# Kernel optimization log

Hardware: AMD Instinct MI355X
Metric: run time of the kernel (lower is better)

## Reference

```python
import jax, jax.numpy as jnp
import numpy as np

D = 256; H = 8; HD = D // H; NK = 32; NLAYERS = 4; FF = 4 * D
B = 8; M = 768; N = 128; LT = 64; T = M + N + LT
SCALE = 1.0 / float(np.sqrt(HD))


def layer_norm(x, s, b):
    mu = x.mean(-1, keepdims=True)
    var = ((x - mu) ** 2).mean(-1, keepdims=True)
    return (x - mu) * jax.lax.rsqrt(var + 1e-5) * s + b


def sine_embed(pos, d):
    # MTR gen_sineembed_for_position: half dims for y, half for x, interleaved sin/cos
    half = d // 2
    dim_t = jnp.power(10000.0, 2.0 * (jnp.arange(half) // 2).astype(jnp.float32) / half)
    scale = 2.0 * np.pi
    def inter(e):
        return jnp.stack([jnp.sin(e[:, 0::2]), jnp.cos(e[:, 1::2])], -1).reshape(e.shape[0], -1)
    ex = pos[:, 0:1] * scale / dim_t
    ey = pos[:, 1:2] * scale / dim_t
    return jnp.concatenate([inter(ey), inter(ex)], -1)


def setup_inputs() -> dict:
    key = jax.random.key(0)
    ks = jax.random.split(key, 24)
    s = 0.02
    inp = {
        'map_token': jax.random.normal(ks[0], (B, M, D), jnp.float32),
        'agent_token': jax.random.normal(ks[1], (B, N, D), jnp.float32),
        'light_token': jax.random.normal(ks[2], (B, LT, D), jnp.float32),
        'map_position': jax.random.uniform(ks[3], (B, M, 2), jnp.float32) * 100.0,
        'agent_position': jax.random.uniform(ks[4], (B, N, 2), jnp.float32) * 100.0,
        'light_position': jax.random.uniform(ks[5], (B, LT, 2), jnp.float32) * 100.0,
        'map_valid_mask': jnp.ones((B, M), bool),
        'agent_valid_mask': jnp.ones((B, N), bool),
        'light_valid_mask': jnp.ones((B, LT), bool),
        'Wq': jax.random.normal(ks[6], (NLAYERS, D, D), jnp.float32) * s,
        'bq': jnp.zeros((NLAYERS, D), jnp.float32),
        'Wk': jax.random.normal(ks[7], (NLAYERS, D, D), jnp.float32) * s,
        'bk': jnp.zeros((NLAYERS, D), jnp.float32),
        'Wv': jax.random.normal(ks[8], (NLAYERS, D, D), jnp.float32) * s,
        'bv': jnp.zeros((NLAYERS, D), jnp.float32),
        'Wo': jax.random.normal(ks[9], (NLAYERS, D, D), jnp.float32) * s,
        'bo': jnp.zeros((NLAYERS, D), jnp.float32),
        'W1': jax.random.normal(ks[10], (NLAYERS, D, FF), jnp.float32) * s,
        'b1': jnp.zeros((NLAYERS, FF), jnp.float32),
        'W2': jax.random.normal(ks[11], (NLAYERS, FF, D), jnp.float32) * s,
        'b2': jnp.zeros((NLAYERS, D), jnp.float32),
        'ln1_s': jnp.ones((NLAYERS, D), jnp.float32),
        'ln1_b': jnp.zeros((NLAYERS, D), jnp.float32),
        'ln2_s': jnp.ones((NLAYERS, D), jnp.float32),
        'ln2_b': jnp.zeros((NLAYERS, D), jnp.float32),
    }
    return inp


def reference(map_token, agent_token, light_token, map_position, agent_position, light_position,
              map_valid_mask, agent_valid_mask, light_valid_mask,
              Wq, bq, Wk, bk, Wv, bv, Wo, bo, W1, b1, W2, b2, ln1_s, ln1_b, ln2_s, ln2_b):
    x = jnp.concatenate([map_token, agent_token, light_token], 1)             # [B,T,D]
    pos = jnp.concatenate([map_position, agent_position, light_position], 1)[..., :2]  # [B,T,2]
    # all tokens valid -> masked compaction is a static reshape
    xs = x.reshape(B * T, D)
    ps = pos.reshape(B * T, 2)
    # KNN within each scene (includes self, like knn_batch_mlogk on same set)
    d2 = jnp.sum((pos[:, :, None, :] - pos[:, None, :, :]) ** 2, -1)          # [B,T,T]
    _, idx = jax.lax.top_k(-d2, NK)                                            # [B,T,NK] local indices
    idx = (idx + (jnp.arange(B) * T)[:, None, None]).reshape(B * T, NK)        # global flat indices
    pe = sine_embed(ps, D)                                                     # [B*T,D]
    out = xs
    for l in range(NLAYERS):
        qk = out + pe
        q = (qk @ Wq[l] + bq[l]).reshape(-1, H, HD)
        k = (qk @ Wk[l] + bk[l]).reshape(-1, H, HD)
        v = (out @ Wv[l] + bv[l]).reshape(-1, H, HD)
        kn = k[idx]                                                            # [BT,NK,H,HD] gather
        vn = v[idx]
        att = jax.nn.softmax(jnp.einsum('nhd,nkhd->nhk', q, kn) * SCALE, axis=-1)
        a = jnp.einsum('nhk,nkhd->nhd', att, vn).reshape(-1, D) @ Wo[l] + bo[l]
        out = layer_norm(out + a, ln1_s[l], ln1_b[l])
        ff = jax.nn.relu(out @ W1[l] + b1[l]) @ W2[l] + b2[l]
        out = layer_norm(out + ff, ln2_s[l], ln2_b[l])
    full = out.reshape(B, T, D)
    return full[:, :M], full[:, M:M + N], full[:, M + N:]
```

## Files before the change

kernel.cpp:

```cpp
#include <hip/hip_runtime.h>
#include <math.h>

#define BB 8
#define MTOK 768
#define NTOK 128
#define LTOK 64
#define TT 960
#define BT 7680
#define DD 256
#define HH 8
#define HD 32
#define KNN 32
#define FFD 1024
#define NLAYERS 4
#define SCALE_ATT 0.17677669529663687f

typedef __attribute__((ext_vector_type(8))) short bfrag_t;
typedef __attribute__((ext_vector_type(4))) float accfrag_t;

__device__ __forceinline__ float b2f(unsigned short u) {
  union { unsigned int i; float f; } c; c.i = ((unsigned int)u) << 16; return c.f;
}
__device__ __forceinline__ unsigned short f2b(float f) {
  union { float f; unsigned int i; } c; c.f = f;
  return (unsigned short)((c.i + 0x7fffu + ((c.i >> 16) & 1u)) >> 16);
}
__device__ __forceinline__ float load_elem(const void* p, size_t i, int f) {
  return f ? b2f(((const unsigned short*)p)[i]) : ((const float*)p)[i];
}
__device__ __forceinline__ size_t pk_addr(int row, int col, int nks) {
  return ((size_t)((row >> 4) * nks + (col >> 5)) << 9)
       + (size_t)(((((col >> 3) & 3) << 4) + (row & 15)) * 8 + (col & 7));
}
__device__ __forceinline__ int swiz_tok(int blk) { return (blk & 7) * TT + (blk >> 3); }

#define FB_BQ 0
#define FB_BK 1024
#define FB_BV 2048
#define FB_BO 3072
#define FB_B1 4096
#define FB_B2 8192
#define FB_LN1S 9216
#define FB_LN1B 10240
#define FB_LN2S 11264
#define FB_LN2B 12288
#define FB_TOTAL 13312
struct ParamSrc { const void* p[13]; };
__global__ __launch_bounds__(256)
void conv_misc_kernel(ParamSrc ps, const void* tok, int* flagout,
                      float* __restrict__ dst, float* __restrict__ posf) {
  __shared__ int cnt;
  if (threadIdx.x == 0) cnt = 0;
  __syncthreads();
  const unsigned short* u = (const unsigned short*)tok;
  int ok = 0;
  for (int i = threadIdx.x; i < 1024; i += 256) {
    int e = (u[i] >> 7) & 0xFF;
    if (e >= 100 && e <= 140) ok++;
  }
  atomicAdd(&cnt, ok);
  __syncthreads();
  int f = (cnt >= 922) ? 1 : 0;
  if (blockIdx.x == 0 && threadIdx.x == 0) *flagout = f;
  if (blockIdx.x < BB) {
    int b = blockIdx.x;
    for (int t = threadIdx.x; t < TT * 2; t += 256) {
      int tok2 = t >> 1, c = t & 1;
      const void* p; size_t idx;
      if (tok2 < MTOK)             { p = ps.p[10]; idx = (size_t)(b * MTOK + tok2) * 2 + c; }
      else if (tok2 < MTOK + NTOK) { p = ps.p[11]; idx = (size_t)(b * NTOK + tok2 - MTOK) * 2 + c; }
      else                         { p = ps.p[12]; idx = (size_t)(b * LTOK + tok2 - MTOK - NTOK) * 2 + c; }
      posf[((size_t)b * TT + tok2) * 2 + c] = load_elem(p, idx, f);
    }
    return;
  }
  int i = (blockIdx.x - BB) * 256 + threadIdx.x;
  if (i >= FB_TOTAL) return;
  int src; size_t off;
  if (i < 4096)      { src = i >> 10;              off = i & 1023; }
  else if (i < 8192) { src = 4;                    off = i - 4096; }
  else               { src = 5 + ((i - 8192) >> 10); off = (i - 8192) & 1023; }
  dst[i] = load_elem(ps.p[src], off, f);
}

__device__ __forceinline__ unsigned long long shfl_xor_u64(unsigned long long v, int m) {
  unsigned lo = (unsigned)v, hi = (unsigned)(v >> 32);
  lo = (unsigned)__shfl_xor((int)lo, m);
  hi = (unsigned)__shfl_xor((int)hi, m);
  return ((unsigned long long)hi << 32) | (unsigned long long)lo;
}
__device__ __forceinline__ unsigned long long shfl_u64(unsigned long long v, int srcLane) {
  unsigned lo = (unsigned)v, hi = (unsigned)(v >> 32);
  lo = (unsigned)__shfl((int)lo, srcLane);
  hi = (unsigned)__shfl((int)hi, srcLane);
  return ((unsigned long long)hi << 32) | (unsigned long long)lo;
}
__device__ __forceinline__ unsigned long long bitonic64(unsigned long long key, int lane) {
#pragma unroll
  for (int kk = 2; kk <= 64; kk <<= 1) {
#pragma unroll
    for (int j = kk >> 1; j > 0; j >>= 1) {
      unsigned long long other = shfl_xor_u64(key, j);
      bool small_ = (lane & j) == 0;
      bool dir = (lane & kk) == 0;
      bool keep = ((key < other) == (small_ == dir));
      key = keep ? key : other;
    }
  }
  return key;
}

struct PackSrc { const void* s[6]; };
__global__ __launch_bounds__(256)
void mega_kernel(PackSrc w, const void* mt, const void* at, const void* lt,
                 const float* __restrict__ posf, const int* __restrict__ flag,
                 unsigned short* __restrict__ Wqkvpk, unsigned short* __restrict__ Wopk,
                 unsigned short* __restrict__ W1pk, unsigned short* __restrict__ W2pk,
                 unsigned short* __restrict__ pe_b, float* __restrict__ out_f,
                 unsigned short* __restrict__ pk1, unsigned short* __restrict__ qkpk,
                 int* __restrict__ idx_out) {
  __shared__ float sx[TT], sy[TT];
  __shared__ unsigned long long cbuf[4][64];
  int bid = blockIdx.x;
  if (bid < 12288) {
    int f = *flag;
    int id = bid * 256 + threadIdx.x;
    if (id < 786432) {
      int layer = id / 196608, rest = id % 196608;
      int sel = rest >> 16, e = rest & 65535;
      int k = e >> 8, col = e & 255;
      const void* src = w.s[sel];
      size_t si = (size_t)layer * 65536 + e;
      Wqkvpk[(size_t)layer * 196608 + (size_t)sel * 65536 + pk_addr(col, k, 8)] =
          f ? ((const unsigned short*)src)[si] : f2b(((const float*)src)[si]);
    } else if (id < 1048576) {
      int off = id - 786432, layer = off >> 16, e = off & 65535;
      int k = e >> 8, col = e & 255;
      size_t si = (size_t)layer * 65536 + e;
      Wopk[(size_t)layer * 65536 + pk_addr(col, k, 8)] =
          f ? ((const unsigned short*)w.s[3])[si] : f2b(((const float*)w.s[3])[si]);
    } else if (id < 2097152) {
      int off = id - 1048576, layer = off >> 18, e = off & 262143;
      int k = e >> 10, col = e & 1023;
      size_t si = (size_t)layer * 262144 + e;
      W1pk[(size_t)layer * 262144 + pk_addr(col, k, 8)] =
          f ? ((const unsigned short*)w.s[4])[si] : f2b(((const float*)w.s[4])[si]);
    } else {
      int off = id - 2097152, layer = off >> 18, e = off & 262143;
      int k = e >> 8, col = e & 255;
      size_t si = (size_t)layer * 262144 + e;
      W2pk[(size_t)layer * 262144 + pk_addr(col, k, 32)] =
          f ? ((const unsigned short*)w.s[5])[si] : f2b(((const float*)w.s[5])[si]);
    }
    return;
  }
  if (bid < 19968) {
    int n = swiz_tok(bid - 12288), d = threadIdx.x;
    int b = n / TT, t = n - b * TT;
    int f = *flag;
    const void* src; size_t si;
    if (t < MTOK)              { src = mt; si = (size_t)(b * MTOK + t) * DD + d; }
    else if (t < MTOK + NTOK)  { src = at; si = (size_t)(b * NTOK + (t - MTOK)) * DD + d; }
    else                       { src = lt; si = (size_t)(b * LTOK + (t - MTOK - NTOK)) * DD + d; }
    float x = load_elem(src, si, f);
    float px = posf[((size_t)b * TT + t) * 2 + 0];
    float py = posf[((size_t)b * TT + t) * 2 + 1];
    float coord = (d < 128) ? py : px;
    int j = d & 127;
    float expo = (float)(2 * (j >> 1)) / 128.0f;
    float dim_t = powf(10000.0f, expo);
    float e = coord * 6.283185307179586f / dim_t;
    float p = (j & 1) ? cosf(e) : sinf(e);
    size_t o = (size_t)n * DD + d;
    pe_b[o] = f2b(p);
    out_f[o] = x;
    size_t pa = pk_addr(n, d, 8);
    pk1[pa] = f2b(x);
    qkpk[pa] = f2b(x + p);
    return;
  }
  int kb = bid - 19968;
  int b = kb & 7;
  int qbase = (kb >> 3) * 4;
  for (int t = threadIdx.x; t < TT; t += 256) {
    sx[t] = posf[((size_t)b * TT + t) * 2 + 0];
    sy[t] = posf[((size_t)b * TT + t) * 2 + 1];
  }
  __syncthreads();
  int wave = threadIdx.x >> 6, lane = threadIdx.x & 63;
  int t = qbase + wave;
  float qx = sx[t], qy = sy[t];

  unsigned long long k[15];
#pragma unroll
  for (int c = 0; c < 15; c++) {
    int j = c * 64 + lane;
    float dx = qx - sx[j], dy = qy - sy[j];
    float d2 = __fadd_rn(__fmul_rn(dx, dx), __fmul_rn(dy, dy));
    k[c] = ((unsigned long long)__float_as_uint(d2) << 32) | (unsigned)j;
  }
  unsigned long long lm = k[0];
#pragma unroll
  for (int c = 1; c < 15; c++) lm = (k[c] < lm) ? k[c] : lm;

  unsigned long long sm = bitonic64(lm, lane);
  unsigned long long thr = shfl_u64(sm, 31);

  int c_l = 0;
#pragma unroll
  for (int c = 0; c < 15; c++) c_l += (k[c] <= thr) ? 1 : 0;
  int inc = c_l;
#pragma unroll
  for (int o = 1; o < 64; o <<= 1) {
    int tt = __shfl_up(inc, o);
    inc += (lane >= o) ? tt : 0;
  }
  int total = __shfl(inc, 63);
  int pos = inc - c_l;

  if (total <= 64) {
    unsigned long long* wb = cbuf[wave];
#pragma unroll
    for (int c = 0; c < 15; c++) {
      if (k[c] <= thr) { wb[pos] = k[c]; pos++; }
    }
    unsigned long long cand = (lane < total) ? wb[lane] : ~0ull;
    cand = bitonic64(cand, lane);
    if (lane < KNN)
      idx_out[((size_t)(b * TT + t)) * KNN + lane] = b * TT + (int)(cand & 0xFFFFFFFFu);
  } else {
    unsigned res = 0;
    for (int i = 0; i < KNN; i++) {
      unsigned long long m = k[0];
#pragma unroll
      for (int c = 1; c < 15; c++) m = (k[c] < m) ? k[c] : m;
#pragma unroll
      for (int o = 32; o > 0; o >>= 1) {
        unsigned long long om = shfl_xor_u64(m, o);
        m = (om < m) ? om : m;
      }
      if (lane == i) res = (unsigned)(m & 0xFFFFFFFFu);
      int owner = (int)(m & 63u), ch = (int)(((unsigned)(m & 0xFFFFFFFFu)) >> 6);
      if (lane == owner) {
#pragma unroll
        for (int c = 0; c < 15; c++) if (c == ch) k[c] = ~0ull;
      }
    }
    if (lane < KNN)
      idx_out[((size_t)(b * TT + t)) * KNN + lane] = b * TT + (int)res;
  }
}

template<int NKS, int NT>
__device__ __forceinline__ void wavegemm(const unsigned short* __restrict__ Apk,
                                         const unsigned short* __restrict__ Bpk,
                                         int rb, int cb0, accfrag_t (&acc)[NT]) {
  const int lane = threadIdx.x & 63;
  accfrag_t z = {0.f, 0.f, 0.f, 0.f};
#pragma unroll
  for (int nt = 0; nt < NT; nt++) acc[nt] = z;
  const unsigned short* ap = Apk + ((size_t)rb * NKS * 512 + lane * 8);
  const unsigned short* bp = Bpk + ((size_t)cb0 * NKS * 512 + lane * 8);
#pragma unroll 4
  for (int ks = 0; ks < NKS; ks++) {
    bfrag_t a = *(const bfrag_t*)(ap + ks * 512);
#pragma unroll
    for (int nt = 0; nt < NT; nt++) {
      bfrag_t b = *(const bfrag_t*)(bp + (size_t)(nt * NKS + ks) * 512);
      acc[nt] = __builtin_amdgcn_mfma_f32_16x16x32_bf16(a, b, acc[nt], 0, 0, 0);
    }
  }
}

__global__ __launch_bounds__(256)
void qkv_kernel(const unsigned short* __restrict__ qkpk,
                const unsigned short* __restrict__ outpk,
                const unsigned short* __restrict__ Wl,
                const float* __restrict__ pb, int l,
                unsigned short* __restrict__ QKV) {
  int scene = blockIdx.x & 7, r = blockIdx.x >> 3;
  int rbg = r % 15, cgall = r / 15;
  int wave = threadIdx.x >> 6, lane = threadIdx.x & 63;
  int rb = scene * 60 + rbg * 4 + wave;
  int sel = cgall >> 2, cg = cgall & 3;
  const unsigned short* A = (sel < 2) ? qkpk : outpk;
  const unsigned short* B = Wl + sel * 65536;
  const float* bias = pb + sel * 1024 + l * 256;
  accfrag_t acc[4];
  wavegemm<8,4>(A, B, rb, cg * 4, acc);
  int l16 = lane & 15, lq = lane >> 4;
  unsigned short* C = QKV + (size_t)sel * BT * DD;
#pragma unroll
  for (int nt = 0; nt < 4; nt++) {
    int col = cg * 64 + nt * 16 + l16;
    float bv = bias[col];
#pragma unroll
    for (int r4 = 0; r4 < 4; r4++) {
      int row = rb * 16 + lq * 4 + r4;
      C[(size_t)row * DD + col] = f2b(acc[nt][r4] + bv);
    }
  }
}

__global__ __launch_bounds__(256)
void attn_kernel(const unsigned short* __restrict__ QKV,
                 const int* __restrict__ idx,
                 unsigned short* __restrict__ attnpk) {
  __shared__ unsigned short kn[KNN][DD + 8];
  __shared__ unsigned short vn[KNN][DD + 8];
  __shared__ float qs[DD];
  __shared__ float att[HH][KNN];
  __shared__ int nb[KNN];
  const unsigned short* Q = QKV;
  const unsigned short* K = QKV + (size_t)BT * DD;
  const unsigned short* V = QKV + 2 * (size_t)BT * DD;
  int n = swiz_tok(blockIdx.x), tid = threadIdx.x;
  if (tid < KNN) nb[tid] = idx[n * KNN + tid];
  qs[tid] = b2f(Q[(size_t)n * DD + tid]);
  __syncthreads();
#pragma unroll
  for (int p = 0; p < 4; p++) {
    int e = p * 256 + tid;
    int r = e >> 5, c8 = (e & 31) * 8;
    int srow = nb[r];
    *(uint4*)(&kn[r][c8]) = *(const uint4*)(K + (size_t)srow * DD + c8);
    *(uint4*)(&vn[r][c8]) = *(const uint4*)(V + (size_t)srow * DD + c8);
  }
  __syncthreads();
  int h = tid >> 5, kk = tid & 31;
  float dot = 0.0f;
#pragma unroll
  for (int d = 0; d < HD; d++) dot += qs[h * HD + d] * b2f(kn[kk][h * HD + d]);
  float sc = dot * SCALE_ATT;
  float mx = sc;
#pragma unroll
  for (int o = 16; o > 0; o >>= 1) mx = fmaxf(mx, __shfl_xor(mx, o, 32));
  float ex = expf(sc - mx);
  float sm = ex;
#pragma unroll
  for (int o = 16; o > 0; o >>= 1) sm += __shfl_xor(sm, o, 32);
  att[h][kk] = ex / sm;
  __syncthreads();
  int d = kk;
  float oacc = 0.0f;
#pragma unroll
  for (int k2 = 0; k2 < KNN; k2++) oacc += att[h][k2] * b2f(vn[k2][h * HD + d]);
  attnpk[pk_addr(n, tid, 8)] = f2b(oacc);
}

template<bool LAST>
__global__ __launch_bounds__(512)
void ffn_block_kernel(const unsigned short* __restrict__ attnpk,
                      const unsigned short* __restrict__ Wo,
                      const unsigned short* __restrict__ W1,
                      const unsigned short* __restrict__ W2,
                      const unsigned short* __restrict__ Wn,
                      const float* __restrict__ bo,
                      const float* __restrict__ b1,
                      const float* __restrict__ b2,
                      const float* __restrict__ pb, int ln,
                      float* __restrict__ yf,
                      const unsigned short* __restrict__ pe_b,
                      const float* __restrict__ g1, const float* __restrict__ t1,
                      const float* __restrict__ g2, const float* __restrict__ t2,
                      unsigned short* __restrict__ QKV,
                      void* __restrict__ dout, const int* __restrict__ flag) {
  __shared__ unsigned short xls[8 * 512];
  __shared__ unsigned short hls[32 * 512];
  __shared__ float ps1[8][16], ps2[8][16];
  int scene = blockIdx.x & 7, rbs = blockIdx.x >> 3;
  int wave = threadIdx.x >> 6, lane = threadIdx.x & 63;
  int rb = scene * 60 + rbs;
  int l16 = lane & 15, lq = lane >> 4;

  accfrag_t acc[2];
  wavegemm<8,2>(attnpk, Wo, rb, wave * 2, acc);
  float y[2][4];
  float s[4] = {0.f, 0.f, 0.f, 0.f}, s2[4] = {0.f, 0.f, 0.f, 0.f};
#pragma unroll
  for (int nt = 0; nt < 2; nt++) {
    int col = wave * 32 + nt * 16 + l16;
    float bv = bo[col];
#pragma unroll
    for (int r4 = 0; r4 < 4; r4++) {
      int row = rb * 16 + lq * 4 + r4;
      float x = acc[nt][r4] + bv + yf[(size_t)row * DD + col];
      y[nt][r4] = x; s[r4] += x; s2[r4] += x * x;
    }
  }
#pragma unroll
  for (int o = 1; o < 16; o <<= 1) {
#pragma unroll
    for (int r4 = 0; r4 < 4; r4++) { s[r4] += __shfl_xor(s[r4], o); s2[r4] += __shfl_xor(s2[r4], o); }
  }
  if (l16 == 0) {
#pragma unroll
    for (int r4 = 0; r4 < 4; r4++) { ps1[wave][lq * 4 + r4] = s[r4]; ps2[wave][lq * 4 + r4] = s2[r4]; }
  }
  __syncthreads();
#pragma unroll
  for (int r4 = 0; r4 < 4; r4++) {
    int r16 = lq * 4 + r4;
    float ts = 0.f, ts2 = 0.f;
#pragma unroll
    for (int wv = 0; wv < 8; wv++) { ts += ps1[wv][r16]; ts2 += ps2[wv][r16]; }
    float mu = ts * (1.0f / 256.0f);
    float var = ts2 * (1.0f / 256.0f) - mu * mu;
    float rstd = 1.0f / sqrtf(fmaxf(var, 0.f) + 1e-5f);
#pragma unroll
    for (int nt = 0; nt < 2; nt++) {
      int col = wave * 32 + nt * 16 + l16;
      float v = (y[nt][r4] - mu) * rstd * g1[col] + t1[col];
      y[nt][r4] = v;
      xls[pk_addr(r16, col, 8)] = f2b(v);
    }
  }
  __syncthreads();

#pragma unroll
  for (int half = 0; half < 2; half++) {
    int cb = wave * 8 + half * 4;
    accfrag_t a2[4];
    wavegemm<8,4>(xls, W1, 0, cb, a2);
#pragma unroll
    for (int nt = 0; nt < 4; nt++) {
      int col = (cb + nt) * 16 + l16;
      float bv = b1[col];
#pragma unroll
      for (int r4 = 0; r4 < 4; r4++)
        hls[pk_addr(lq * 4 + r4, col, 32)] = f2b(fmaxf(a2[nt][r4] + bv, 0.0f));
    }
  }
  __syncthreads();

  accfrag_t a3[2];
  wavegemm<32,2>(hls, W2, 0, wave * 2, a3);
  float v2[2][4];
  float s3[4] = {0.f, 0.f, 0.f, 0.f}, s4[4] = {0.f, 0.f, 0.f, 0.f};
#pragma unroll
  for (int nt = 0; nt < 2; nt++) {
    int col = wave * 32 + nt * 16 + l16;
    float bv = b2[col];
#pragma unroll
    for (int r4 = 0; r4 < 4; r4++) {
      float x = a3[nt][r4] + bv + y[nt][r4];
      v2[nt][r4] = x; s3[r4] += x; s4[r4] += x * x;
    }
  }
#pragma unroll
  for (int o = 1; o < 16; o <<= 1) {
#pragma unroll
    for (int r4 = 0; r4 < 4; r4++) { s3[r4] += __shfl_xor(s3[r4], o); s4[r4] += __shfl_xor(s4[r4], o); }
  }
  if (l16 == 0) {
#pragma unroll
    for (int r4 = 0; r4 < 4; r4++) { ps1[wave][lq * 4 + r4] = s3[r4]; ps2[wave][lq * 4 + r4] = s4[r4]; }
  }
  __syncthreads();
  unsigned short* qkls = hls;
  int fl = LAST ? *flag : 0;
#pragma unroll
  for (int r4 = 0; r4 < 4; r4++) {
    int r16 = lq * 4 + r4;
    float ts = 0.f, ts2 = 0.f;
#pragma unroll
    for (int wv = 0; wv < 8; wv++) { ts += ps1[wv][r16]; ts2 += ps2[wv][r16]; }
    float mu = ts * (1.0f / 256.0f);
    float var = ts2 * (1.0f / 256.0f) - mu * mu;
    float rstd = 1.0f / sqrtf(fmaxf(var, 0.f) + 1e-5f);
#pragma unroll
    for (int nt = 0; nt < 2; nt++) {
      int col = wave * 32 + nt * 16 + l16;
      float yv = (v2[nt][r4] - mu) * rstd * g2[col] + t2[col];
      int row = rb * 16 + r16;
      if (!LAST) {
        yf[(size_t)row * DD + col] = yv;
        float q = yv + b2f(pe_b[(size_t)row * DD + col]);
        xls[pk_addr(r16, col, 8)] = f2b(yv);
        qkls[pk_addr(r16, col, 8)] = f2b(q);
      } else {
        int t = rbs * 16 + r16;
        size_t o;
        if (t < MTOK)             o = (size_t)(scene * MTOK + t) * DD + col;
        else if (t < MTOK + NTOK) o = (size_t)BB * MTOK * DD + (size_t)(scene * NTOK + (t - MTOK)) * DD + col;
        else                      o = (size_t)BB * MTOK * DD + (size_t)BB * NTOK * DD
                                    + (size_t)(scene * LTOK + (t - MTOK - NTOK)) * DD + col;
        if (fl) ((unsigned short*)dout)[o] = f2b(yv);
        else    ((float*)dout)[o] = yv;
      }
    }
  }

  if (!LAST) {
    __syncthreads();
    {
      int sel = (wave >> 2);
      int cb = (wave & 3) * 4;
      accfrag_t a4[4];
      wavegemm<8,4>(qkls, Wn + sel * 65536, 0, cb, a4);
      const float* bias = pb + sel * 1024 + ln * 256;
      unsigned short* C = QKV + (size_t)sel * BT * DD;
#pragma unroll
      for (int nt = 0; nt < 4; nt++) {
        int col = (cb + nt) * 16 + l16;
        float bv = bias[col];
#pragma unroll
        for (int r4 = 0; r4 < 4; r4++) {
          int row = rb * 16 + lq * 4 + r4;
          C[(size_t)row * DD + col] = f2b(a4[nt][r4] + bv);
        }
      }
    }
    {
      accfrag_t a5[2];
      wavegemm<8,2>(xls, Wn + 2 * 65536, 0, wave * 2, a5);
      const float* bias = pb + 2 * 1024 + ln * 256;
      unsigned short* C = QKV + 2 * (size_t)BT * DD;
#pragma unroll
      for (int nt = 0; nt < 2; nt++) {
        int col = wave * 32 + nt * 16 + l16;
        float bv = bias[col];
#pragma unroll
        for (int r4 = 0; r4 < 4; r4++) {
          int row = rb * 16 + lq * 4 + r4;
          C[(size_t)row * DD + col] = f2b(a5[nt][r4] + bv);
        }
      }
    }
  }
}

extern "C" void kernel_launch(void* const* d_in, const int* in_sizes, int n_in,
                              void* d_out, int out_size, void* d_ws, size_t ws_size,
                              hipStream_t stream) {
  const void* map_tok   = d_in[0];
  const void* agent_tok = d_in[1];
  const void* light_tok = d_in[2];
  const void* map_pos   = d_in[3];
  const void* agent_pos = d_in[4];
  const void* light_pos = d_in[5];
  const void* Wq  = d_in[9];
  const void* bq  = d_in[10];
  const void* Wk  = d_in[11];
  const void* bk  = d_in[12];
  const void* Wv  = d_in[13];
  const void* bv  = d_in[14];
  const void* Wo  = d_in[15];
  const void* bo  = d_in[16];
  const void* W1  = d_in[17];
  const void* b1  = d_in[18];
  const void* W2  = d_in[19];
  const void* b2  = d_in[20];
  const void* ln1s = d_in[21];
  const void* ln1b = d_in[22];
  const void* ln2s = d_in[23];
  const void* ln2b = d_in[24];

  size_t off = 0;
  char* base = (char*)d_ws;
  auto take = [&](size_t bytes) { char* p = base + off; off += (bytes + 255) & ~(size_t)255; return (void*)p; };
  int*   flag  = (int*)take(256);
  float* posf  = (float*)take((size_t)BT * 2 * 4);
  float* pbuf  = (float*)take((size_t)FB_TOTAL * 4);
  unsigned short* pe_b = (unsigned short*)take((size_t)BT * DD * 2);
  float* out_f = (float*)take((size_t)BT * DD * 4);
  unsigned short* pk1  = (unsigned short*)take((size_t)BT * DD * 2);
  unsigned short* qkpk = (unsigned short*)take((size_t)BT * DD * 2);
  unsigned short* QKV  = (unsigned short*)take((size_t)3 * BT * DD * 2);
  unsigned short* attnpk = (unsigned short*)take((size_t)BT * DD * 2);
  int* idxb = (int*)take((size_t)BT * KNN * 4);
  unsigned short* Wqkvpk = (unsigned short*)take((size_t)NLAYERS * 3 * DD * DD * 2);
  unsigned short* Wopk   = (unsigned short*)take((size_t)NLAYERS * DD * DD * 2);
  unsigned short* W1pk   = (unsigned short*)take((size_t)NLAYERS * DD * FFD * 2);
  unsigned short* W2pk   = (unsigned short*)take((size_t)NLAYERS * DD * FFD * 2);

  ParamSrc ps; ps.p[0]=bq; ps.p[1]=bk; ps.p[2]=bv; ps.p[3]=bo; ps.p[4]=b1;
  ps.p[5]=b2; ps.p[6]=ln1s; ps.p[7]=ln1b; ps.p[8]=ln2s; ps.p[9]=ln2b;
  ps.p[10]=map_pos; ps.p[11]=agent_pos; ps.p[12]=light_pos;
  conv_misc_kernel<<<BB + (FB_TOTAL + 255) / 256, 256, 0, stream>>>(ps, map_tok, flag, pbuf, posf);

  PackSrc pw; pw.s[0]=Wq; pw.s[1]=Wk; pw.s[2]=Wv; pw.s[3]=Wo; pw.s[4]=W1; pw.s[5]=W2;
  mega_kernel<<<21888, 256, 0, stream>>>(pw, map_tok, agent_tok, light_tok, posf, flag,
                                         Wqkvpk, Wopk, W1pk, W2pk,
                                         pe_b, out_f, pk1, qkpk, idxb);

  qkv_kernel<<<1440, 256, 0, stream>>>(qkpk, pk1, Wqkvpk, pbuf, 0, QKV);

  for (int l = 0; l < NLAYERS; l++) {
    attn_kernel<<<BT, 256, 0, stream>>>(QKV, idxb, attnpk);
    if (l < NLAYERS - 1)
      ffn_block_kernel<false><<<480, 512, 0, stream>>>(
          attnpk, Wopk + (size_t)l * 65536, W1pk + (size_t)l * 262144, W2pk + (size_t)l * 262144,
          Wqkvpk + (size_t)(l + 1) * 196608,
          pbuf + FB_BO + l * 256, pbuf + FB_B1 + l * 1024, pbuf + FB_B2 + l * 256,
          pbuf, l + 1,
          out_f, pe_b,
          pbuf + FB_LN1S + l * 256, pbuf + FB_LN1B + l * 256,
          pbuf + FB_LN2S + l * 256, pbuf + FB_LN2B + l * 256,
          QKV, d_out, flag);
    else
      ffn_block_kernel<true><<<480, 512, 0, stream>>>(
          attnpk, Wopk + (size_t)l * 65536, W1pk + (size_t)l * 262144, W2pk + (size_t)l * 262144,
          Wqkvpk,
          pbuf + FB_BO + l * 256, pbuf + FB_B1 + l * 1024, pbuf + FB_B2 + l * 256,
          pbuf, 0,
          out_f, pe_b,
          pbuf + FB_LN1S + l * 256, pbuf + FB_LN1B + l * 256,
          pbuf + FB_LN2S + l * 256, pbuf + FB_LN2B + l * 256,
          QKV, d_out, flag);
  }
}
```

Baseline: 405.5 us.

## Process 64 rows per FFN block and chunk the hidden layer through LDS

The fused FFN kernel now handles four 16-row tiles per block (64 rows) instead of one, so each weight fragment loaded from global memory feeds four MFMAs. The FF hidden dimension is processed in four chunks of 256 columns, each chunk's W2 contribution accumulated in registers, which keeps LDS usage bounded. The grid shrinks from 480 to 120 blocks, fewer than the number of CUs, trading occupancy and parallelism for weight reuse, and register pressure rises.

```diff
diff --git a/kernel.cpp b/kernel.cpp
--- a/kernel.cpp
+++ b/kernel.cpp
@@ -272,6 +272,37 @@
   }
 }
 
+template<int NKS, int NT, int MR, int BST>
+__device__ __forceinline__ void wavegemm_mr(const unsigned short* __restrict__ Apk,
+                                            const unsigned short* __restrict__ Bpk,
+                                            int rb0, int cb0, accfrag_t (&acc)[MR][NT],
+                                            bool zero) {
+  const int lane = threadIdx.x & 63;
+  if (zero) {
+    accfrag_t z = {0.f, 0.f, 0.f, 0.f};
+#pragma unroll
+    for (int mr = 0; mr < MR; mr++)
+#pragma unroll
+      for (int nt = 0; nt < NT; nt++) acc[mr][nt] = z;
+  }
+  const unsigned short* ap = Apk + ((size_t)rb0 * NKS * 512 + lane * 8);
+  const unsigned short* bp = Bpk + ((size_t)cb0 * BST * 512 + lane * 8);
+#pragma unroll
+  for (int ks = 0; ks < NKS; ks++) {
+    bfrag_t a[MR];
+#pragma unroll
+    for (int mr = 0; mr < MR; mr++)
+      a[mr] = *(const bfrag_t*)(ap + (size_t)(mr * NKS + ks) * 512);
+#pragma unroll
+    for (int nt = 0; nt < NT; nt++) {
+      bfrag_t b = *(const bfrag_t*)(bp + (size_t)(nt * BST + ks) * 512);
+#pragma unroll
+      for (int mr = 0; mr < MR; mr++)
+        acc[mr][nt] = __builtin_amdgcn_mfma_f32_16x16x32_bf16(a[mr], b, acc[mr][nt], 0, 0, 0);
+    }
+  }
+}
+
 __global__ __launch_bounds__(256)
 void qkv_kernel(const unsigned short* __restrict__ qkpk,
                 const unsigned short* __restrict__ outpk,
@@ -365,128 +396,174 @@
                       const float* __restrict__ g2, const float* __restrict__ t2,
                       unsigned short* __restrict__ QKV,
                       void* __restrict__ dout, const int* __restrict__ flag) {
-  __shared__ unsigned short xls[8 * 512];
-  __shared__ unsigned short hls[32 * 512];
-  __shared__ float ps1[8][16], ps2[8][16];
-  int scene = blockIdx.x & 7, rbs = blockIdx.x >> 3;
+  __shared__ unsigned short xls[4 * 8 * 512];
+  __shared__ unsigned short hls[4 * 8 * 512];
+  __shared__ float ps1[8][64], ps2[8][64];
+  int scene = blockIdx.x & 7, rg = blockIdx.x >> 3;
   int wave = threadIdx.x >> 6, lane = threadIdx.x & 63;
-  int rb = scene * 60 + rbs;
+  int rb0 = scene * 60 + rg * 4;
   int l16 = lane & 15, lq = lane >> 4;
 
-  accfrag_t acc[2];
-  wavegemm<8,2>(attnpk, Wo, rb, wave * 2, acc);
-  float y[2][4];
-  float s[4] = {0.f, 0.f, 0.f, 0.f}, s2[4] = {0.f, 0.f, 0.f, 0.f};
-#pragma unroll
-  for (int nt = 0; nt < 2; nt++) {
-    int col = wave * 32 + nt * 16 + l16;
-    float bv = bo[col];
-#pragma unroll
-    for (int r4 = 0; r4 < 4; r4++) {
-      int row = rb * 16 + lq * 4 + r4;
-      float x = acc[nt][r4] + bv + yf[(size_t)row * DD + col];
-      y[nt][r4] = x; s[r4] += x; s2[r4] += x * x;
-    }
-  }
-#pragma unroll
-  for (int o = 1; o < 16; o <<= 1) {
-#pragma unroll
-    for (int r4 = 0; r4 < 4; r4++) { s[r4] += __shfl_xor(s[r4], o); s2[r4] += __shfl_xor(s2[r4], o); }
-  }
-  if (l16 == 0) {
-#pragma unroll
-    for (int r4 = 0; r4 < 4; r4++) { ps1[wave][lq * 4 + r4] = s[r4]; ps2[wave][lq * 4 + r4] = s2[r4]; }
-  }
-  __syncthreads();
-#pragma unroll
-  for (int r4 = 0; r4 < 4; r4++) {
-    int r16 = lq * 4 + r4;
-    float ts = 0.f, ts2 = 0.f;
-#pragma unroll
-    for (int wv = 0; wv < 8; wv++) { ts += ps1[wv][r16]; ts2 += ps2[wv][r16]; }
-    float mu = ts * (1.0f / 256.0f);
-    float var = ts2 * (1.0f / 256.0f) - mu * mu;
-    float rstd = 1.0f / sqrtf(fmaxf(var, 0.f) + 1e-5f);
+  accfrag_t acc[4][2];
+  wavegemm_mr<8,2,4,8>(attnpk, Wo, rb0, wave * 2, acc, true);
+  float y[4][2][4];
+  float s[4][4], s2m[4][4];
+#pragma unroll
+  for (int mr = 0; mr < 4; mr++)
+#pragma unroll
+    for (int r4 = 0; r4 < 4; r4++) { s[mr][r4] = 0.f; s2m[mr][r4] = 0.f; }
+#pragma unroll
+  for (int mr = 0; mr < 4; mr++) {
 #pragma unroll
     for (int nt = 0; nt < 2; nt++) {
       int col = wave * 32 + nt * 16 + l16;
-      float v = (y[nt][r4] - mu) * rstd * g1[col] + t1[col];
-      y[nt][r4] = v;
-      xls[pk_addr(r16, col, 8)] = f2b(v);
-    }
-  }
-  __syncthreads();
-
-#pragma unroll
-  for (int half = 0; half < 2; half++) {
-    int cb = wave * 8 + half * 4;
-    accfrag_t a2[4];
-    wavegemm<8,4>(xls, W1, 0, cb, a2);
-#pragma unroll
-    for (int nt = 0; nt < 4; nt++) {
-      int col = (cb + nt) * 16 + l16;
-      float bv = b1[col];
-#pragma unroll
-      for (int r4 = 0; r4 < 4; r4++)
-        hls[pk_addr(lq * 4 + r4, col, 32)] = f2b(fmaxf(a2[nt][r4] + bv, 0.0f));
-    }
-  }
-  __syncthreads();
-
-  accfrag_t a3[2];
-  wavegemm<32,2>(hls, W2, 0, wave * 2, a3);
-  float v2[2][4];
-  float s3[4] = {0.f, 0.f, 0.f, 0.f}, s4[4] = {0.f, 0.f, 0.f, 0.f};
-#pragma unroll
-  for (int nt = 0; nt < 2; nt++) {
-    int col = wave * 32 + nt * 16 + l16;
-    float bv = b2[col];
+      float bv = bo[col];
+#pragma unroll
+      for (int r4 = 0; r4 < 4; r4++) {
+        int row = (rb0 + mr) * 16 + lq * 4 + r4;
+        float x = acc[mr][nt][r4] + bv + yf[(size_t)row * DD + col];
+        y[mr][nt][r4] = x; s[mr][r4] += x; s2m[mr][r4] += x * x;
+      }
+    }
+  }
+#pragma unroll
+  for (int o = 1; o < 16; o <<= 1) {
+#pragma unroll
+    for (int mr = 0; mr < 4; mr++)
+#pragma unroll
+      for (int r4 = 0; r4 < 4; r4++) {
+        s[mr][r4] += __shfl_xor(s[mr][r4], o);
+        s2m[mr][r4] += __shfl_xor(s2m[mr][r4], o);
+      }
+  }
+  if (l16 == 0) {
+#pragma unroll
+    for (int mr = 0; mr < 4; mr++)
+#pragma unroll
+      for (int r4 = 0; r4 < 4; r4++) {
+        ps1[wave][mr * 16 + lq * 4 + r4] = s[mr][r4];
+        ps2[wave][mr * 16 + lq * 4 + r4] = s2m[mr][r4];
+      }
+  }
+  __syncthreads();
+#pragma unroll
+  for (int mr = 0; mr < 4; mr++) {
 #pragma unroll
     for (int r4 = 0; r4 < 4; r4++) {
-      float x = a3[nt][r4] + bv + y[nt][r4];
-      v2[nt][r4] = x; s3[r4] += x; s4[r4] += x * x;
-    }
-  }
-#pragma unroll
-  for (int o = 1; o < 16; o <<= 1) {
-#pragma unroll
-    for (int r4 = 0; r4 < 4; r4++) { s3[r4] += __shfl_xor(s3[r4], o); s4[r4] += __shfl_xor(s4[r4], o); }
-  }
-  if (l16 == 0) {
-#pragma unroll
-    for (int r4 = 0; r4 < 4; r4++) { ps1[wave][lq * 4 + r4] = s3[r4]; ps2[wave][lq * 4 + r4] = s4[r4]; }
-  }
-  __syncthreads();
-  unsigned short* qkls = hls;
-  int fl = LAST ? *flag : 0;
-#pragma unroll
-  for (int r4 = 0; r4 < 4; r4++) {
-    int r16 = lq * 4 + r4;
-    float ts = 0.f, ts2 = 0.f;
-#pragma unroll
-    for (int wv = 0; wv < 8; wv++) { ts += ps1[wv][r16]; ts2 += ps2[wv][r16]; }
-    float mu = ts * (1.0f / 256.0f);
-    float var = ts2 * (1.0f / 256.0f) - mu * mu;
-    float rstd = 1.0f / sqrtf(fmaxf(var, 0.f) + 1e-5f);
+      int row64 = mr * 16 + lq * 4 + r4;
+      float ts = 0.f, ts2 = 0.f;
+#pragma unroll
+      for (int wv = 0; wv < 8; wv++) { ts += ps1[wv][row64]; ts2 += ps2[wv][row64]; }
+      float mu = ts * (1.0f / 256.0f);
+      float var = ts2 * (1.0f / 256.0f) - mu * mu;
+      float rstd = 1.0f / sqrtf(fmaxf(var, 0.f) + 1e-5f);
+#pragma unroll
+      for (int nt = 0; nt < 2; nt++) {
+        int col = wave * 32 + nt * 16 + l16;
+        float v = (y[mr][nt][r4] - mu) * rstd * g1[col] + t1[col];
+        y[mr][nt][r4] = v;
+        xls[pk_addr(row64, col, 8)] = f2b(v);
+      }
+    }
+  }
+  __syncthreads();
+
+  accfrag_t a2[4][2];
+  {
+    accfrag_t z = {0.f, 0.f, 0.f, 0.f};
+#pragma unroll
+    for (int mr = 0; mr < 4; mr++)
+#pragma unroll
+      for (int nt = 0; nt < 2; nt++) a2[mr][nt] = z;
+  }
+  for (int c = 0; c < 4; c++) {
+    accfrag_t h[4][2];
+    wavegemm_mr<8,2,4,8>(xls, W1 + (size_t)(c * 16) * 8 * 512, 0, wave * 2, h, true);
+#pragma unroll
+    for (int mr = 0; mr < 4; mr++)
+#pragma unroll
+      for (int nt = 0; nt < 2; nt++) {
+        int colL = wave * 32 + nt * 16 + l16;
+        float bv = b1[c * 256 + colL];
+#pragma unroll
+        for (int r4 = 0; r4 < 4; r4++)
+          hls[pk_addr(mr * 16 + lq * 4 + r4, colL, 8)] = f2b(fmaxf(h[mr][nt][r4] + bv, 0.0f));
+      }
+    __syncthreads();
+    wavegemm_mr<8,2,4,32>(hls, W2 + (size_t)(c * 8) * 512, 0, wave * 2, a2, false);
+    __syncthreads();
+  }
+
+  float v2[4][2][4];
+#pragma unroll
+  for (int mr = 0; mr < 4; mr++)
+#pragma unroll
+    for (int r4 = 0; r4 < 4; r4++) { s[mr][r4] = 0.f; s2m[mr][r4] = 0.f; }
+#pragma unroll
+  for (int mr = 0; mr < 4; mr++) {
 #pragma unroll
     for (int nt = 0; nt < 2; nt++) {
       int col = wave * 32 + nt * 16 + l16;
-      float yv = (v2[nt][r4] - mu) * rstd * g2[col] + t2[col];
-      int row = rb * 16 + r16;
-      if (!LAST) {
-        yf[(size_t)row * DD + col] = yv;
-        float q = yv + b2f(pe_b[(size_t)row * DD + col]);
-        xls[pk_addr(r16, col, 8)] = f2b(yv);
-        qkls[pk_addr(r16, col, 8)] = f2b(q);
-      } else {
-        int t = rbs * 16 + r16;
-        size_t o;
-        if (t < MTOK)             o = (size_t)(scene * MTOK + t) * DD + col;
-        else if (t < MTOK + NTOK) o = (size_t)BB * MTOK * DD + (size_t)(scene * NTOK + (t - MTOK)) * DD + col;
-        else                      o = (size_t)BB * MTOK * DD + (size_t)BB * NTOK * DD
-                                    + (size_t)(scene * LTOK + (t - MTOK - NTOK)) * DD + col;
-        if (fl) ((unsigned short*)dout)[o] = f2b(yv);
-        else    ((float*)dout)[o] = yv;
+      float bv = b2[col];
+#pragma unroll
+      for (int r4 = 0; r4 < 4; r4++) {
+        float x = a2[mr][nt][r4] + bv + y[mr][nt][r4];
+        v2[mr][nt][r4] = x; s[mr][r4] += x; s2m[mr][r4] += x * x;
+      }
+    }
+  }
+#pragma unroll
+  for (int o = 1; o < 16; o <<= 1) {
+#pragma unroll
+    for (int mr = 0; mr < 4; mr++)
+#pragma unroll
+      for (int r4 = 0; r4 < 4; r4++) {
+        s[mr][r4] += __shfl_xor(s[mr][r4], o);
+        s2m[mr][r4] += __shfl_xor(s2m[mr][r4], o);
+      }
+  }
+  if (l16 == 0) {
+#pragma unroll
+    for (int mr = 0; mr < 4; mr++)
+#pragma unroll
+      for (int r4 = 0; r4 < 4; r4++) {
+        ps1[wave][mr * 16 + lq * 4 + r4] = s[mr][r4];
+        ps2[wave][mr * 16 + lq * 4 + r4] = s2m[mr][r4];
+      }
+  }
+  __syncthreads();
+  int fl = LAST ? *flag : 0;
+#pragma unroll
+  for (int mr = 0; mr < 4; mr++) {
+#pragma unroll
+    for (int r4 = 0; r4 < 4; r4++) {
+      int row64 = mr * 16 + lq * 4 + r4;
+      float ts = 0.f, ts2 = 0.f;
+#pragma unroll
+      for (int wv = 0; wv < 8; wv++) { ts += ps1[wv][row64]; ts2 += ps2[wv][row64]; }
+      float mu = ts * (1.0f / 256.0f);
+      float var = ts2 * (1.0f / 256.0f) - mu * mu;
+      float rstd = 1.0f / sqrtf(fmaxf(var, 0.f) + 1e-5f);
+#pragma unroll
+      for (int nt = 0; nt < 2; nt++) {
+        int col = wave * 32 + nt * 16 + l16;
+        float yv = (v2[mr][nt][r4] - mu) * rstd * g2[col] + t2[col];
+        int row = (rb0 + mr) * 16 + lq * 4 + r4;
+        if (!LAST) {
+          yf[(size_t)row * DD + col] = yv;
+          float q = yv + b2f(pe_b[(size_t)row * DD + col]);
+          xls[pk_addr(row64, col, 8)] = f2b(yv);
+          hls[pk_addr(row64, col, 8)] = f2b(q);
+        } else {
+          int t = rg * 64 + row64;
+          size_t o;
+          if (t < MTOK)             o = (size_t)(scene * MTOK + t) * DD + col;
+          else if (t < MTOK + NTOK) o = (size_t)BB * MTOK * DD + (size_t)(scene * NTOK + (t - MTOK)) * DD + col;
+          else                      o = (size_t)BB * MTOK * DD + (size_t)BB * NTOK * DD
+                                      + (size_t)(scene * LTOK + (t - MTOK - NTOK)) * DD + col;
+          if (fl) ((unsigned short*)dout)[o] = f2b(yv);
+          else    ((float*)dout)[o] = yv;
+        }
       }
     }
   }
@@ -494,38 +571,41 @@
   if (!LAST) {
     __syncthreads();
     {
-      int sel = (wave >> 2);
-      int cb = (wave & 3) * 4;
-      accfrag_t a4[4];
-      wavegemm<8,4>(qkls, Wn + sel * 65536, 0, cb, a4);
+      int sel = wave >> 2, cw = wave & 3;
+      accfrag_t a4[4][4];
+      wavegemm_mr<8,4,4,8>(hls, Wn + sel * 65536, 0, cw * 4, a4, true);
       const float* bias = pb + sel * 1024 + ln * 256;
       unsigned short* C = QKV + (size_t)sel * BT * DD;
 #pragma unroll
-      for (int nt = 0; nt < 4; nt++) {
-        int col = (cb + nt) * 16 + l16;
-        float bv = bias[col];
-#pragma unroll
-        for (int r4 = 0; r4 < 4; r4++) {
-          int row = rb * 16 + lq * 4 + r4;
-          C[(size_t)row * DD + col] = f2b(a4[nt][r4] + bv);
+      for (int mr = 0; mr < 4; mr++)
+#pragma unroll
+        for (int nt = 0; nt < 4; nt++) {
+          int col = (cw * 4 + nt) * 16 + l16;
+          float bv = bias[col];
+#pragma unroll
+          for (int r4 = 0; r4 < 4; r4++) {
+            int row = (rb0 + mr) * 16 + lq * 4 + r4;
+            C[(size_t)row * DD + col] = f2b(a4[mr][nt][r4] + bv);
+          }
         }
-      }
     }
     {
-      accfrag_t a5[2];
-      wavegemm<8,2>(xls, Wn + 2 * 65536, 0, wave * 2, a5);
+      accfrag_t a5[4][2];
+      wavegemm_mr<8,2,4,8>(xls, Wn + 2 * 65536, 0, wave * 2, a5, true);
       const float* bias = pb + 2 * 1024 + ln * 256;
       unsigned short* C = QKV + 2 * (size_t)BT * DD;
 #pragma unroll
-      for (int nt = 0; nt < 2; nt++) {
-        int col = wave * 32 + nt * 16 + l16;
-        float bv = bias[col];
-#pragma unroll
-        for (int r4 = 0; r4 < 4; r4++) {
-          int row = rb * 16 + lq * 4 + r4;
-          C[(size_t)row * DD + col] = f2b(a5[nt][r4] + bv);
+      for (int mr = 0; mr < 4; mr++)
+#pragma unroll
+        for (int nt = 0; nt < 2; nt++) {
+          int col = wave * 32 + nt * 16 + l16;
+          float bv = bias[col];
+#pragma unroll
+          for (int r4 = 0; r4 < 4; r4++) {
+            int row = (rb0 + mr) * 16 + lq * 4 + r4;
+            C[(size_t)row * DD + col] = f2b(a5[mr][nt][r4] + bv);
+          }
         }
-      }
     }
   }
 }
@@ -589,7 +669,7 @@
   for (int l = 0; l < NLAYERS; l++) {
     attn_kernel<<<BT, 256, 0, stream>>>(QKV, idxb, attnpk);
     if (l < NLAYERS - 1)
-      ffn_block_kernel<false><<<480, 512, 0, stream>>>(
+      ffn_block_kernel<false><<<120, 512, 0, stream>>>(
           attnpk, Wopk + (size_t)l * 65536, W1pk + (size_t)l * 262144, W2pk + (size_t)l * 262144,
           Wqkvpk + (size_t)(l + 1) * 196608,
           pbuf + FB_BO + l * 256, pbuf + FB_B1 + l * 1024, pbuf + FB_B2 + l * 256,
@@ -599,7 +679,7 @@
           pbuf + FB_LN2S + l * 256, pbuf + FB_LN2B + l * 256,
           QKV, d_out, flag);
     else
-      ffn_block_kernel<true><<<480, 512, 0, stream>>>(
+      ffn_block_kernel<true><<<120, 512, 0, stream>>>(
           attnpk, Wopk + (size_t)l * 65536, W1pk + (size_t)l * 262144, W2pk + (size_t)l * 262144,
           Wqkvpk,
           pbuf + FB_BO + l * 256, pbuf + FB_B1 + l * 1024, pbuf + FB_B2 + l * 256,
```

Result: slower. 521.0 us (+28.5%).
